# Kernel optimization log

Hardware: AMD Instinct MI355X
Metric: run time of the kernel (lower is better)

Reference implementation:

```python
import jax, jax.numpy as jnp
import numpy as np

NUM_LEVELS = 4
RADIUS = 4


def _bilinear_zeros(img, x, y):
    """Bilinear sample img (N,H,W) at absolute pixel coords x,y (N,S,S),
    zeros padding outside, matching torch grid_sample(align_corners=True,
    padding_mode='zeros') with absolute->normalized->absolute roundtrip."""
    N, H, W = img.shape
    x0 = jnp.floor(x); y0 = jnp.floor(y)
    x1 = x0 + 1.0;     y1 = y0 + 1.0
    wx1 = x - x0; wx0 = 1.0 - wx1
    wy1 = y - y0; wy0 = 1.0 - wy1
    flat = img.reshape(N, H * W)

    def gather(xi, yi):
        valid = (xi >= 0) & (xi <= W - 1) & (yi >= 0) & (yi <= H - 1)
        xc = jnp.clip(xi, 0, W - 1).astype(jnp.int32)
        yc = jnp.clip(yi, 0, H - 1).astype(jnp.int32)
        idx = (yc * W + xc).reshape(N, -1)
        v = jnp.take_along_axis(flat, idx, axis=1).reshape(xi.shape)
        return jnp.where(valid, v, jnp.zeros((), img.dtype))

    return (wy0 * wx0 * gather(x0, y0) + wy0 * wx1 * gather(x1, y0)
            + wy1 * wx0 * gather(x0, y1) + wy1 * wx1 * gather(x1, y1))


def _avg_pool2(v):
    N, H, W = v.shape
    return v.reshape(N, H // 2, 2, W // 2, 2).mean(axis=(2, 4))


def setup_inputs() -> dict:
    key = jax.random.key(0)
    k1, k2, k3 = jax.random.split(key, 3)
    B, M, C, H, W = 2, 4096, 256, 64, 64
    fmap1 = jax.random.normal(k1, (B, M, C), dtype=jnp.float32)
    fmap2 = jax.random.normal(k2, (B, C, H, W), dtype=jnp.float32)
    u = jax.random.uniform(k3, (B, M, 2), dtype=jnp.float32)
    centroids_coords = u * jnp.array([W - 1, H - 1], dtype=jnp.float32)
    return {"fmap1": fmap1, "fmap2": fmap2, "centroids_coords": centroids_coords}


def reference(fmap1, fmap2, centroids_coords):
    B, M, C = fmap1.shape
    _, _, H, W = fmap2.shape
    side = 2 * RADIUS + 1

    # correlation volume: (B, M, H, W) -> (B*M, H, W)
    corr = jnp.einsum('bmc,bchw->bmhw', fmap1, fmap2).reshape(B * M, H, W)

    d = jnp.arange(-RADIUS, RADIUS + 1, dtype=centroids_coords.dtype)
    di, dj = jnp.meshgrid(d, d, indexing='ij')
    delta = jnp.stack([di, dj], axis=-1)  # (S, S, 2): ch0 = x-offset, ch1 = y-offset

    c = centroids_coords.reshape(B * M, 1, 1, 2)
    vol = corr
    feats = []
    for lvl in range(NUM_LEVELS):
        sc = c + delta                        # (B*M, S, S, 2)
        sampled = _bilinear_zeros(vol, sc[..., 0], sc[..., 1])
        feats.append(sampled.reshape(B, M, side * side))
        c = c / 2.0
        if lvl < NUM_LEVELS - 1:
            vol = _avg_pool2(vol)
    # (B, M, num_levels*S*S) -> (B, out_channels, M)
    return jnp.concatenate(feats, axis=-1).transpose(0, 2, 1)
```

## Files before the change

kernel.cpp:

```cpp
#include <hip/hip_runtime.h>
#include <stdint.h>
#include <stddef.h>

static constexpr int Bb = 2;
static constexpr int Mq = 4096;
static constexpr int Cc = 256;
static constexpr int Hh = 64, Ww = 64;
static constexpr int Np = Hh * Ww;
static constexpr int RAD = 4;
static constexpr int SIDE = 2 * RAD + 1;
static constexpr int KPL = SIDE * SIDE;
static constexpr int NLVL = 4;
static constexpr int KTOT = NLVL * KPL;

static constexpr size_t L1BUF_B  = 0;
static constexpr size_t WINBUF_B = (size_t)Bb * Mq * 1024 * 4;
static constexpr size_t ABF_B    = WINBUF_B + (size_t)Bb * Mq * 100 * 4;
static constexpr size_t BT_B     = ABF_B + (size_t)Bb * Mq * Cc * 2;

typedef float floatx4 __attribute__((ext_vector_type(4)));
typedef short shortx8 __attribute__((ext_vector_type(8)));

union BfPack {
    shortx8 v;
    unsigned short u[8];
};

__device__ __forceinline__ unsigned short f2bf(float f) {
    unsigned int x = __float_as_uint(f);
    x += 0x7fffu + ((x >> 16) & 1u);
    return (unsigned short)(x >> 16);
}

__device__ __forceinline__ void gll16(const void* g, void* l) {
    __builtin_amdgcn_global_load_lds(
        (const __attribute__((address_space(1))) unsigned int*)g,
        (__attribute__((address_space(3))) unsigned int*)l, 16, 0, 0);
}

__global__ __launch_bounds__(256)
void cvt_a_kernel(const float* __restrict__ in, unsigned short* __restrict__ out)
{
    const int t = blockIdx.x * blockDim.x + threadIdx.x;
    const float4 v0 = *(const float4*)(in + (size_t)t * 8);
    const float4 v1 = *(const float4*)(in + (size_t)t * 8 + 4);
    BfPack p;
    p.u[0] = f2bf(v0.x); p.u[1] = f2bf(v0.y);
    p.u[2] = f2bf(v0.z); p.u[3] = f2bf(v0.w);
    p.u[4] = f2bf(v1.x); p.u[5] = f2bf(v1.y);
    p.u[6] = f2bf(v1.z); p.u[7] = f2bf(v1.w);
    *(shortx8*)(out + (size_t)t * 8) = p.v;
}

__global__ __launch_bounds__(256)
void cvt_bt_kernel(const float* __restrict__ in, unsigned short* __restrict__ out)
{
    __shared__ float tile[64 * 65];
    const int p0 = blockIdx.x * 64;
    const int c0 = blockIdx.y * 64;
    const int b  = blockIdx.z;
    const int tid = threadIdx.x;

    const int pl = tid & 63;
    const int cb = tid >> 6;
#pragma unroll
    for (int it = 0; it < 16; ++it) {
        const int cl = it * 4 + cb;
        tile[cl * 65 + pl] = in[((size_t)(b * Cc + c0 + cl)) * Np + p0 + pl];
    }
    __syncthreads();

    const int cg = (tid & 7) * 8;
#pragma unroll
    for (int it = 0; it < 2; ++it) {
        const int pw = it * 32 + (tid >> 3);
        BfPack p;
#pragma unroll
        for (int u = 0; u < 8; ++u)
            p.u[u] = f2bf(tile[(cg + u) * 65 + pw]);
        *(shortx8*)(out + ((size_t)(b * Np + p0 + pw)) * Cc + c0 + cg) = p.v;
    }
}

__global__ __launch_bounds__(256)
void corr_gemm_pool_kernel(const unsigned short* __restrict__ Abf,
                           const unsigned short* __restrict__ Bt,
                           const float* __restrict__ cent,
                           float* __restrict__ l1buf,
                           float* __restrict__ winbuf)
{
    __shared__ union {
        struct { unsigned short la[128 * 32]; unsigned short lb[128 * 32]; } t;
        float corrT[32 * 130];
    } sm;
    __shared__ int qx0s[128], qy0s[128];

    const int b    = blockIdx.z;
    const int bm0  = blockIdx.y * 128;
    const int bx   = blockIdx.x;
    const int bn0  = bx * 128;
    const int tid  = threadIdx.x;
    const int lane = tid & 63;
    const int wave = tid >> 6;
    const int lane15 = lane & 15;
    const int quad   = lane >> 4;
    const int wm = (wave >> 1) * 64;
    const int wn = (wave & 1) * 64;

    if (tid < 128) {
        const float cx = cent[(size_t)(b * Mq + bm0 + tid) * 2 + 0];
        const float cy = cent[(size_t)(b * Mq + bm0 + tid) * 2 + 1];
        qx0s[tid] = (int)floorf(cx) - RAD;
        qy0s[tid] = (int)floorf(cy) - RAD;
    }

    unsigned short* la = sm.t.la;
    unsigned short* lb = sm.t.lb;

    const int lrow = lane >> 2;
    const int lkg  = (lane & 3) * 8;
    const unsigned short* aptr = Abf + (size_t)(b * Mq + bm0 + wave * 16 + lrow) * Cc + lkg;
    const unsigned short* bptr = Bt  + (size_t)(b * Np + bn0 + wave * 16 + lrow) * Cc + lkg;

    floatx4 acc[4][4];
#pragma unroll
    for (int i = 0; i < 4; ++i)
#pragma unroll
        for (int j = 0; j < 4; ++j)
            acc[i][j] = floatx4{0.0f, 0.0f, 0.0f, 0.0f};

    for (int k0 = 0; k0 < Cc; k0 += 32) {
        __syncthreads();
        gll16(aptr + k0,            &la[wave * 512]);
        gll16(aptr + 64 * Cc + k0,  &la[2048 + wave * 512]);
        gll16(bptr + k0,            &lb[wave * 512]);
        gll16(bptr + 64 * Cc + k0,  &lb[2048 + wave * 512]);
        __syncthreads();

        shortx8 af[4], bf[4];
#pragma unroll
        for (int i = 0; i < 4; ++i)
            af[i] = *(const shortx8*)&la[(wm + i * 16 + lane15) * 32 + quad * 8];
#pragma unroll
        for (int j = 0; j < 4; ++j)
            bf[j] = *(const shortx8*)&lb[(wn + j * 16 + lane15) * 32 + quad * 8];
#pragma unroll
        for (int i = 0; i < 4; ++i)
#pragma unroll
            for (int j = 0; j < 4; ++j)
                acc[i][j] = __builtin_amdgcn_mfma_f32_16x16x32_bf16(
                    af[i], bf[j], acc[i][j], 0, 0, 0);
    }

    float* corrT = sm.corrT;
    const int m_local = tid >> 3;
    const int xi      = tid & 7;
#pragma unroll
    for (int c = 0; c < 4; ++c) {
        __syncthreads();
        if ((wave >> 1) == (c >> 1)) {
#pragma unroll
            for (int ii = 0; ii < 2; ++ii) {
                const int i = 2 * (c & 1) + ii;
#pragma unroll
                for (int j = 0; j < 4; ++j) {
#pragma unroll
                    for (int reg = 0; reg < 4; ++reg) {
                        const int rl = ii * 16 + quad * 4 + reg;
                        const int n  = wn + j * 16 + lane15;
                        corrT[rl * 130 + n] = acc[i][j][reg];
                    }
                }
            }
        }
        __syncthreads();

        const int mg = 32 * c + m_local;
        const size_t gq = (size_t)(b * Mq + bm0 + mg);
        const float* T = &corrT[m_local * 130];

#pragma unroll
        for (int k = 0; k < 4; ++k) {
            const int c1 = xi + 8 * k;
            const float v = 0.25f * (T[2 * c1] + T[2 * c1 + 1]
                                   + T[64 + 2 * c1] + T[64 + 2 * c1 + 1]);
            l1buf[gq * 1024 + bx * 32 + c1] = v;
        }

        const int x0w = qx0s[mg];
        const int y0w = qy0s[mg];
#pragma unroll
        for (int par = 0; par < 2; ++par) {
            const int wy = 2 * bx + par - y0w;
            if (wy >= 0 && wy < 10) {
#pragma unroll
                for (int t = 0; t < 2; ++t) {
                    const int wx = xi + t * 8;
                    if (wx < 10) {
                        const int x = x0w + wx;
                        if (x >= 0 && x < Ww)
                            winbuf[gq * 100 + wy * 10 + wx] = T[par * 64 + x];
                    }
                }
            }
        }
    }
}

__global__ __launch_bounds__(256)
void pyr_sample_kernel(const float* __restrict__ cent,
                       const float* __restrict__ l1buf,
                       const float* __restrict__ winbuf,
                       float* __restrict__ out)
{
    __shared__ float l1[8][1024];
    __shared__ float l2[8][256];
    __shared__ float l3[8][64];
    __shared__ float win0[8][100];
    __shared__ float qcx[8], qcy[8];
    __shared__ int   qx0[8], qy0[8];

    const int tid = threadIdx.x;
    const int b   = blockIdx.x >> 9;
    const int m0  = (blockIdx.x & 511) * 8;
    const size_t gq0 = (size_t)(b * Mq + m0);

    if (tid < 8) {
        const float cx = cent[(gq0 + tid) * 2 + 0];
        const float cy = cent[(gq0 + tid) * 2 + 1];
        qcx[tid] = cx; qcy[tid] = cy;
        qx0[tid] = (int)floorf(cx) - RAD;
        qy0[tid] = (int)floorf(cy) - RAD;
    }

#pragma unroll
    for (int it = 0; it < 8; ++it) {
        const int v = it * 256 + tid;
        const int q = v >> 8;
        const int o = v & 255;
        *(float4*)&l1[q][o * 4] = *(const float4*)&l1buf[(gq0 + q) * 1024 + o * 4];
    }
    if (tid < 200) {
        const int q = tid / 25;
        const int o = tid - q * 25;
        *(float4*)&win0[q][o * 4] = *(const float4*)&winbuf[(gq0 + q) * 100 + o * 4];
    }
    __syncthreads();

#pragma unroll
    for (int i = 0; i < 8; ++i) {
        const int idx = i * 256 + tid;
        const int q = idx >> 8;
        const int c = idx & 255;
        const int cy2 = c >> 4, cx2 = c & 15;
        const float* s = &l1[q][(2 * cy2) * 32 + 2 * cx2];
        l2[q][c] = 0.25f * (s[0] + s[1] + s[32] + s[33]);
    }
    __syncthreads();
#pragma unroll
    for (int i = 0; i < 2; ++i) {
        const int idx = i * 256 + tid;
        const int q = idx >> 6;
        const int c = idx & 63;
        const int cy3 = c >> 3, cx3 = c & 7;
        const float* s = &l2[q][(2 * cy3) * 16 + 2 * cx3];
        l3[q][c] = 0.25f * (s[0] + s[1] + s[16] + s[17]);
    }
    __syncthreads();

    for (int i = 0; i < 11; ++i) {
        const int idx = i * 256 + tid;
        if (idx >= KTOT * 8) break;
        const int q  = idx & 7;
        const int kk = idx >> 3;
        const int lvl = kk / KPL;
        const int r   = kk - lvl * KPL;
        const int di  = r / SIDE;
        const int dj  = r - di * SIDE;

        const int w = Ww >> lvl;
        const float scale = 1.0f / (float)(1 << lvl);
        const float x = qcx[q] * scale + (float)(di - RAD);
        const float y = qcy[q] * scale + (float)(dj - RAD);

        const float x0f = floorf(x), y0f = floorf(y);
        const float wx1 = x - x0f, wx0 = 1.0f - wx1;
        const float wy1 = y - y0f, wy0 = 1.0f - wy1;
        const float fmx = (float)(w - 1);
        const bool vx0 = (x0f >= 0.0f) && (x0f <= fmx);
        const bool vx1 = (x0f + 1.0f >= 0.0f) && (x0f + 1.0f <= fmx);
        const bool vy0 = (y0f >= 0.0f) && (y0f <= fmx);
        const bool vy1 = (y0f + 1.0f >= 0.0f) && (y0f + 1.0f <= fmx);

        const int ix0 = (int)x0f, iy0 = (int)y0f;

        const float* buf;
        int stride, ox, oy;
        if (lvl == 0)      { buf = win0[q]; stride = 10; ox = qx0[q]; oy = qy0[q]; }
        else if (lvl == 1) { buf = l1[q];   stride = 32; ox = 0; oy = 0; }
        else if (lvl == 2) { buf = l2[q];   stride = 16; ox = 0; oy = 0; }
        else               { buf = l3[q];   stride =  8; ox = 0; oy = 0; }

        const int cx0 = ix0 - ox, cx1 = ix0 + 1 - ox;
        const int cy0r = iy0 - oy, cy1r = iy0 + 1 - oy;
        const float g00 = (vx0 && vy0) ? buf[cy0r * stride + cx0] : 0.0f;
        const float g10 = (vx1 && vy0) ? buf[cy0r * stride + cx1] : 0.0f;
        const float g01 = (vx0 && vy1) ? buf[cy1r * stride + cx0] : 0.0f;
        const float g11 = (vx1 && vy1) ? buf[cy1r * stride + cx1] : 0.0f;

        out[((size_t)b * KTOT + kk) * Mq + m0 + q] =
            wy0 * (wx0 * g00 + wx1 * g10) + wy1 * (wx0 * g01 + wx1 * g11);
    }
}

extern "C" void kernel_launch(void* const* d_in, const int* in_sizes, int n_in,
                              void* d_out, int out_size, void* d_ws, size_t ws_size,
                              hipStream_t stream)
{
    const float* fmap1 = (const float*)d_in[0];
    const float* fmap2 = (const float*)d_in[1];
    const float* cent  = (const float*)d_in[2];
    char* ws = (char*)d_ws;
    float* l1buf  = (float*)(ws + L1BUF_B);
    float* winbuf = (float*)(ws + WINBUF_B);
    unsigned short* Abf = (unsigned short*)(ws + ABF_B);
    unsigned short* Bt  = (unsigned short*)(ws + BT_B);
    float* out = (float*)d_out;

    cvt_a_kernel<<<Bb * Mq * Cc / (8 * 256), 256, 0, stream>>>(fmap1, Abf);
    dim3 tgrid(Np / 64, Cc / 64, Bb);
    cvt_bt_kernel<<<tgrid, 256, 0, stream>>>(fmap2, Bt);

    dim3 ggrid(Np / 128, Mq / 128, Bb);
    corr_gemm_pool_kernel<<<ggrid, 256, 0, stream>>>(Abf, Bt, cent, l1buf, winbuf);

    const int nblk = Bb * Mq / 8;
    pyr_sample_kernel<<<nblk, 256, 0, stream>>>(cent, l1buf, winbuf, out);
}
```

Measured before the change: 128.7 us.

## Load GEMM fragments directly from global into registers with prefetch

```diff
diff --git a/kernel.cpp b/kernel.cpp
--- a/kernel.cpp
+++ b/kernel.cpp
@@ -32,12 +32,6 @@
     return (unsigned short)(x >> 16);
 }
 
-__device__ __forceinline__ void gll16(const void* g, void* l) {
-    __builtin_amdgcn_global_load_lds(
-        (const __attribute__((address_space(1))) unsigned int*)g,
-        (__attribute__((address_space(3))) unsigned int*)l, 16, 0, 0);
-}
-
 __global__ __launch_bounds__(256)
 void cvt_a_kernel(const float* __restrict__ in, unsigned short* __restrict__ out)
 {
@@ -89,10 +83,7 @@
                            float* __restrict__ l1buf,
                            float* __restrict__ winbuf)
 {
-    __shared__ union {
-        struct { unsigned short la[128 * 32]; unsigned short lb[128 * 32]; } t;
-        float corrT[32 * 130];
-    } sm;
+    __shared__ float corrT[32 * 130];
     __shared__ int qx0s[128], qy0s[128];
 
     const int b    = blockIdx.z;
@@ -114,13 +105,14 @@
         qy0s[tid] = (int)floorf(cy) - RAD;
     }
 
-    unsigned short* la = sm.t.la;
-    unsigned short* lb = sm.t.lb;
-
-    const int lrow = lane >> 2;
-    const int lkg  = (lane & 3) * 8;
-    const unsigned short* aptr = Abf + (size_t)(b * Mq + bm0 + wave * 16 + lrow) * Cc + lkg;
-    const unsigned short* bptr = Bt  + (size_t)(b * Np + bn0 + wave * 16 + lrow) * Cc + lkg;
+    const unsigned short* arow[4];
+    const unsigned short* brow[4];
+#pragma unroll
+    for (int i = 0; i < 4; ++i)
+        arow[i] = Abf + (size_t)(b * Mq + bm0 + wm + i * 16 + lane15) * Cc + quad * 8;
+#pragma unroll
+    for (int j = 0; j < 4; ++j)
+        brow[j] = Bt + (size_t)(b * Np + bn0 + wn + j * 16 + lane15) * Cc + quad * 8;
 
     floatx4 acc[4][4];
 #pragma unroll
@@ -129,30 +121,31 @@
         for (int j = 0; j < 4; ++j)
             acc[i][j] = floatx4{0.0f, 0.0f, 0.0f, 0.0f};
 
+    shortx8 af[4], bf[4], afn[4], bfn[4];
+#pragma unroll
+    for (int i = 0; i < 4; ++i) af[i] = *(const shortx8*)(arow[i]);
+#pragma unroll
+    for (int j = 0; j < 4; ++j) bf[j] = *(const shortx8*)(brow[j]);
+
     for (int k0 = 0; k0 < Cc; k0 += 32) {
-        __syncthreads();
-        gll16(aptr + k0,            &la[wave * 512]);
-        gll16(aptr + 64 * Cc + k0,  &la[2048 + wave * 512]);
-        gll16(bptr + k0,            &lb[wave * 512]);
-        gll16(bptr + 64 * Cc + k0,  &lb[2048 + wave * 512]);
-        __syncthreads();
-
-        shortx8 af[4], bf[4];
-#pragma unroll
-        for (int i = 0; i < 4; ++i)
-            af[i] = *(const shortx8*)&la[(wm + i * 16 + lane15) * 32 + quad * 8];
-#pragma unroll
-        for (int j = 0; j < 4; ++j)
-            bf[j] = *(const shortx8*)&lb[(wn + j * 16 + lane15) * 32 + quad * 8];
+        if (k0 + 32 < Cc) {
+#pragma unroll
+            for (int i = 0; i < 4; ++i) afn[i] = *(const shortx8*)(arow[i] + k0 + 32);
+#pragma unroll
+            for (int j = 0; j < 4; ++j) bfn[j] = *(const shortx8*)(brow[j] + k0 + 32);
+        }
 #pragma unroll
         for (int i = 0; i < 4; ++i)
 #pragma unroll
             for (int j = 0; j < 4; ++j)
                 acc[i][j] = __builtin_amdgcn_mfma_f32_16x16x32_bf16(
                     af[i], bf[j], acc[i][j], 0, 0, 0);
-    }
-
-    float* corrT = sm.corrT;
+#pragma unroll
+        for (int i = 0; i < 4; ++i) af[i] = afn[i];
+#pragma unroll
+        for (int j = 0; j < 4; ++j) bf[j] = bfn[j];
+    }
+
     const int m_local = tid >> 3;
     const int xi      = tid & 7;
 #pragma unroll
```

Result: slower. 162.3 us (+26.1%).

## Double-buffer GEMM LDS staging and merge the two conversion kernels

Applied to the files above, without the earlier changes.

```diff
diff --git a/kernel.cpp b/kernel.cpp
--- a/kernel.cpp
+++ b/kernel.cpp
@@ -39,34 +39,34 @@
 }
 
 __global__ __launch_bounds__(256)
-void cvt_a_kernel(const float* __restrict__ in, unsigned short* __restrict__ out)
-{
-    const int t = blockIdx.x * blockDim.x + threadIdx.x;
-    const float4 v0 = *(const float4*)(in + (size_t)t * 8);
-    const float4 v1 = *(const float4*)(in + (size_t)t * 8 + 4);
-    BfPack p;
-    p.u[0] = f2bf(v0.x); p.u[1] = f2bf(v0.y);
-    p.u[2] = f2bf(v0.z); p.u[3] = f2bf(v0.w);
-    p.u[4] = f2bf(v1.x); p.u[5] = f2bf(v1.y);
-    p.u[6] = f2bf(v1.z); p.u[7] = f2bf(v1.w);
-    *(shortx8*)(out + (size_t)t * 8) = p.v;
-}
-
-__global__ __launch_bounds__(256)
-void cvt_bt_kernel(const float* __restrict__ in, unsigned short* __restrict__ out)
+void cvt_kernel(const float* __restrict__ f1, const float* __restrict__ f2,
+                unsigned short* __restrict__ Abf, unsigned short* __restrict__ Bt)
 {
     __shared__ float tile[64 * 65];
-    const int p0 = blockIdx.x * 64;
-    const int c0 = blockIdx.y * 64;
-    const int b  = blockIdx.z;
     const int tid = threadIdx.x;
+    if (blockIdx.x < 1024) {
+        const int t = blockIdx.x * 256 + tid;
+        const float4 v0 = *(const float4*)(f1 + (size_t)t * 8);
+        const float4 v1 = *(const float4*)(f1 + (size_t)t * 8 + 4);
+        BfPack p;
+        p.u[0] = f2bf(v0.x); p.u[1] = f2bf(v0.y);
+        p.u[2] = f2bf(v0.z); p.u[3] = f2bf(v0.w);
+        p.u[4] = f2bf(v1.x); p.u[5] = f2bf(v1.y);
+        p.u[6] = f2bf(v1.z); p.u[7] = f2bf(v1.w);
+        *(shortx8*)(Abf + (size_t)t * 8) = p.v;
+        return;
+    }
+    const int bid = blockIdx.x - 1024;
+    const int p0 = (bid & 63) * 64;
+    const int c0 = ((bid >> 6) & 3) * 64;
+    const int b  = bid >> 8;
 
     const int pl = tid & 63;
     const int cb = tid >> 6;
 #pragma unroll
     for (int it = 0; it < 16; ++it) {
         const int cl = it * 4 + cb;
-        tile[cl * 65 + pl] = in[((size_t)(b * Cc + c0 + cl)) * Np + p0 + pl];
+        tile[cl * 65 + pl] = f2[((size_t)(b * Cc + c0 + cl)) * Np + p0 + pl];
     }
     __syncthreads();
 
@@ -78,7 +78,7 @@
 #pragma unroll
         for (int u = 0; u < 8; ++u)
             p.u[u] = f2bf(tile[(cg + u) * 65 + pw]);
-        *(shortx8*)(out + ((size_t)(b * Np + p0 + pw)) * Cc + c0 + cg) = p.v;
+        *(shortx8*)(Bt + ((size_t)(b * Np + p0 + pw)) * Cc + c0 + cg) = p.v;
     }
 }
 
@@ -90,8 +90,8 @@
                            float* __restrict__ winbuf)
 {
     __shared__ union {
-        struct { unsigned short la[128 * 32]; unsigned short lb[128 * 32]; } t;
-        float corrT[32 * 130];
+        unsigned short stage[2][2][128 * 32];
+        float corrT[32 * 131];
     } sm;
     __shared__ int qx0s[128], qy0s[128];
 
@@ -114,9 +114,6 @@
         qy0s[tid] = (int)floorf(cy) - RAD;
     }
 
-    unsigned short* la = sm.t.la;
-    unsigned short* lb = sm.t.lb;
-
     const int lrow = lane >> 2;
     const int lkg  = (lane & 3) * 8;
     const unsigned short* aptr = Abf + (size_t)(b * Mq + bm0 + wave * 16 + lrow) * Cc + lkg;
@@ -129,14 +126,23 @@
         for (int j = 0; j < 4; ++j)
             acc[i][j] = floatx4{0.0f, 0.0f, 0.0f, 0.0f};
 
-    for (int k0 = 0; k0 < Cc; k0 += 32) {
+    gll16(aptr,           &sm.stage[0][0][wave * 512]);
+    gll16(aptr + 64 * Cc, &sm.stage[0][0][2048 + wave * 512]);
+    gll16(bptr,           &sm.stage[0][1][wave * 512]);
+    gll16(bptr + 64 * Cc, &sm.stage[0][1][2048 + wave * 512]);
+
+    for (int k0 = 0; k0 < 8; ++k0) {
         __syncthreads();
-        gll16(aptr + k0,            &la[wave * 512]);
-        gll16(aptr + 64 * Cc + k0,  &la[2048 + wave * 512]);
-        gll16(bptr + k0,            &lb[wave * 512]);
-        gll16(bptr + 64 * Cc + k0,  &lb[2048 + wave * 512]);
-        __syncthreads();
-
+        if (k0 < 7) {
+            const int nb = (k0 + 1) & 1;
+            const int ko = (k0 + 1) * 32;
+            gll16(aptr + ko,           &sm.stage[nb][0][wave * 512]);
+            gll16(aptr + 64 * Cc + ko, &sm.stage[nb][0][2048 + wave * 512]);
+            gll16(bptr + ko,           &sm.stage[nb][1][wave * 512]);
+            gll16(bptr + 64 * Cc + ko, &sm.stage[nb][1][2048 + wave * 512]);
+        }
+        const unsigned short* la = sm.stage[k0 & 1][0];
+        const unsigned short* lb = sm.stage[k0 & 1][1];
         shortx8 af[4], bf[4];
 #pragma unroll
         for (int i = 0; i < 4; ++i)
@@ -168,7 +174,7 @@
                     for (int reg = 0; reg < 4; ++reg) {
                         const int rl = ii * 16 + quad * 4 + reg;
                         const int n  = wn + j * 16 + lane15;
-                        corrT[rl * 130 + n] = acc[i][j][reg];
+                        corrT[rl * 131 + n] = acc[i][j][reg];
                     }
                 }
             }
@@ -177,7 +183,7 @@
 
         const int mg = 32 * c + m_local;
         const size_t gq = (size_t)(b * Mq + bm0 + mg);
-        const float* T = &corrT[m_local * 130];
+        const float* T = &corrT[m_local * 131];
 
 #pragma unroll
         for (int k = 0; k < 4; ++k) {
@@ -327,9 +333,7 @@
     unsigned short* Bt  = (unsigned short*)(ws + BT_B);
     float* out = (float*)d_out;
 
-    cvt_a_kernel<<<Bb * Mq * Cc / (8 * 256), 256, 0, stream>>>(fmap1, Abf);
-    dim3 tgrid(Np / 64, Cc / 64, Bb);
-    cvt_bt_kernel<<<tgrid, 256, 0, stream>>>(fmap2, Bt);
+    cvt_kernel<<<1536, 256, 0, stream>>>(fmap1, fmap2, Abf, Bt);
 
     dim3 ggrid(Np / 128, Mq / 128, Bb);
     corr_gemm_pool_kernel<<<ggrid, 256, 0, stream>>>(Abf, Bt, cent, l1buf, winbuf);
```

Result: faster. 123.5 us (-4.0%).
